# Kernel optimization log

Measured on AMD Instinct MI355X. Metric: run time of the kernel, lower is better.

Reference implementation:

```python
import jax, jax.numpy as jnp
import numpy as np

DIM = 1024
NUM_HEAD = 16
N_IMG = 64


def _linear_params(key, scale=0.02):
    kw, kb = jax.random.split(key)
    W = jax.random.normal(kw, (DIM, DIM), jnp.float32) * scale
    b = jax.random.normal(kb, (DIM,), jnp.float32) * scale
    return W, b


def setup_inputs() -> dict:
    key = jax.random.key(0)
    ks = jax.random.split(key, 5)
    # ragged per-image instance counts: 128..254, deterministic, sum = 12224
    lens = (128 + 2 * np.arange(N_IMG)).astype(np.int64)
    N = int(lens.sum())  # 12224
    x = jax.random.normal(ks[0], (N, DIM), jnp.float32)
    Wq, bq = _linear_params(ks[1])
    Wk, bk = _linear_params(ks[2])
    Wv, bv = _linear_params(ks[3])
    Wu, bu = _linear_params(ks[4])
    return {"x": x, "Wq": Wq, "bq": bq, "Wk": Wk, "bk": bk,
            "Wv": Wv, "bv": bv, "Wu": Wu, "bu": bu,
            "num_inst_per_image": jnp.asarray(lens)}


def _segment_layout(num_inst_per_image):
    # static (int) metadata -> numpy; returns padded gather idx, key mask, unpad idx
    lens = np.asarray(num_inst_per_image)
    B = lens.shape[0]
    L = int(lens.max())
    offsets = np.concatenate([[0], np.cumsum(lens)[:-1]])
    pos = offsets[:, None] + np.arange(L)[None, :]           # [B, L] flat positions
    valid = np.arange(L)[None, :] < lens[:, None]            # [B, L]
    gather_idx = jnp.asarray(np.where(valid, pos, 0))        # safe gather
    flat_take = jnp.asarray(np.flatnonzero(valid.ravel()))   # [N] unpad (row-major = segment order)
    return gather_idx, jnp.asarray(valid), flat_take, B, L


def reference(x, Wq, bq, Wk, bk, Wv, bv, Wu, bu, num_inst_per_image):
    gather_idx, valid, flat_take, B, L = _segment_layout(num_inst_per_image)
    N, C = x.shape
    H = NUM_HEAD
    D = C // H
    # global QKV projections on the flat batch (as in the torch module)
    q = (x @ Wq + bq)[gather_idx].reshape(B, L, H, D)
    k = (x @ Wk + bk)[gather_idx].reshape(B, L, H, D)
    v = (x @ Wv + bv)[gather_idx].reshape(B, L, H, D)
    scale = 1.0 / np.sqrt(C)  # note: original divides by sqrt(C), not sqrt(head_dim)
    attn = jnp.einsum('bqhd,bkhd->bhqk', q, k) * scale       # [B, H, L, L]
    bias = jnp.where(valid[:, None, None, :], 0.0, -jnp.inf)  # mask padded keys
    attn = jax.nn.softmax(attn + bias, axis=-1)
    out = jnp.einsum('bhqk,bkhd->bqhd', attn, v).reshape(B * L, C)
    out = out[flat_take]                                      # unpad back to [N, C]
    return out @ Wu + bu
```

## Files before the change

### kernel.cpp

```cpp
#include <hip/hip_runtime.h>
#include <hip/hip_bf16.h>
#include <math.h>

#define DIMC 1024
#define NHEAD 16
#define HDIM 64
#define MPAD 12288

using bf16x8 = __attribute__((ext_vector_type(8))) short;
using f32x4  = __attribute__((ext_vector_type(4))) float;
using f32x16 = __attribute__((ext_vector_type(16))) float;

__device__ inline ushort f2bf(float f) {
    uint u = __float_as_uint(f);
    u += 0x7fffu + ((u >> 16) & 1u);
    return (ushort)(u >> 16);
}
__device__ inline float bf2f(ushort h) { return __uint_as_float(((uint)h) << 16); }

__device__ inline uint pkbf(float a, float b) {
    __hip_bfloat162 t = __float22bfloat162_rn(float2{a, b});
    return *reinterpret_cast<uint*>(&t);
}

__device__ inline void gload_lds16(const ushort* g, ushort* l) {
    __builtin_amdgcn_global_load_lds(
        (const __attribute__((address_space(1))) uint*)g,
        (__attribute__((address_space(3))) uint*)l, 16, 0, 0);
}

__global__ __launch_bounds__(512, 2) void gemm192(
    const ushort* __restrict__ A, const ushort* __restrict__ Bt,
    const float* __restrict__ bq, const float* __restrict__ bk,
    const float* __restrict__ bv,
    ushort* __restrict__ qb, ushort* __restrict__ kb, ushort* __restrict__ vb,
    int M)
{
    __shared__ ushort lds[2][(256 + 192) * 64];

    const int bid = blockIdx.x;
    const int xcd = bid & 7;
    const int j   = bid >> 3;
    const int mt  = xcd * 6 + (j % 6);
    const int nt  = j / 6;
    const int row0 = mt * 256;
    const int col0 = nt * 192;

    const int t512 = threadIdx.x;
    const int w    = t512 >> 6;
    const int lane = t512 & 63;
    const int wm   = w >> 2;
    const int wn   = w & 3;
    const int l15  = lane & 15;
    const int kh   = lane >> 4;

    auto stage = [&](int buf, int kt, int mat, int relRow) {
        const int o   = relRow * 128 + lane * 16;
        const int row = o >> 7;
        const int kb_ = (o & 127) ^ ((row & 7) << 4);
        const ushort* src = (mat ? Bt + (size_t)(col0 + row) * DIMC
                                 : A  + (size_t)(row0 + row) * DIMC)
                            + kt * 64 + (kb_ >> 1);
        gload_lds16(src, &lds[buf][0] + mat * (256 * 64) + relRow * 64);
    };
    auto rdA = [&](int buf, int qr, int fr, int ks) -> bf16x8 {
        const int row = wm * 128 + qr * 64 + fr * 16 + l15;
        const int ad  = (row * 128 + ks * 64 + kh * 16) ^ ((row & 7) << 4);
        return *(const bf16x8*)(&lds[buf][0] + (ad >> 1));
    };
    auto rdB = [&](int buf, int n, int ks) -> bf16x8 {
        const int row = wn * 48 + n * 16 + l15;
        const int ad  = (row * 128 + ks * 64 + kh * 16) ^ ((row & 7) << 4);
        return *(const bf16x8*)(&lds[buf][256 * 64] + (ad >> 1));
    };

    f32x4 acc[8][3] = {};
    bf16x8 af[4][2];
    bf16x8 bf[3][2];

    stage(0, 0, 0, wm * 128 + wn * 16);
    stage(0, 0, 0, wm * 128 + wn * 16 + 8);
    stage(0, 0, 1, wn * 48 + wm * 16);
    stage(0, 0, 1, wn * 48 + wm * 16 + 8);
    stage(0, 0, 1, wn * 48 + 32 + wm * 8);
    stage(0, 0, 0, wm * 128 + 64 + wn * 16);
    stage(0, 0, 0, wm * 128 + 64 + wn * 16 + 8);

    const int NT = DIMC / 64;
    for (int t = 0; t < NT; ++t) {
        const int cur = t & 1;
        const int nxt = cur ^ 1;
        const int tn  = (t + 1 < NT) ? (t + 1) : (NT - 1);

        asm volatile("s_waitcnt vmcnt(3)" ::: "memory");
        __builtin_amdgcn_s_barrier();
        __builtin_amdgcn_sched_barrier(0);
        #pragma unroll
        for (int fr = 0; fr < 4; ++fr)
            #pragma unroll
            for (int ks = 0; ks < 2; ++ks)
                af[fr][ks] = rdA(cur, 0, fr, ks);
        #pragma unroll
        for (int n = 0; n < 2; ++n)
            #pragma unroll
            for (int ks = 0; ks < 2; ++ks)
                bf[n][ks] = rdB(cur, n, ks);
        stage(nxt, tn, 0, wm * 128 + wn * 16);
        stage(nxt, tn, 0, wm * 128 + wn * 16 + 8);
        stage(nxt, tn, 1, wn * 48 + wm * 16);
        stage(nxt, tn, 1, wn * 48 + wm * 16 + 8);
        __builtin_amdgcn_s_setprio(1);
        #pragma unroll
        for (int fr = 0; fr < 4; ++fr)
            #pragma unroll
            for (int n = 0; n < 2; ++n)
                #pragma unroll
                for (int ks = 0; ks < 2; ++ks)
                    acc[fr][n] = __builtin_amdgcn_mfma_f32_16x16x32_bf16(
                        af[fr][ks], bf[n][ks], acc[fr][n], 0, 0, 0);
        __builtin_amdgcn_s_setprio(0);

        asm volatile("s_waitcnt vmcnt(6)" ::: "memory");
        __builtin_amdgcn_s_barrier();
        __builtin_amdgcn_sched_barrier(0);
        #pragma unroll
        for (int ks = 0; ks < 2; ++ks)
            bf[2][ks] = rdB(cur, 2, ks);
        stage(nxt, tn, 1, wn * 48 + 32 + wm * 8);
        __builtin_amdgcn_s_setprio(1);
        #pragma unroll
        for (int fr = 0; fr < 4; ++fr)
            #pragma unroll
            for (int ks = 0; ks < 2; ++ks)
                acc[fr][2] = __builtin_amdgcn_mfma_f32_16x16x32_bf16(
                    af[fr][ks], bf[2][ks], acc[fr][2], 0, 0, 0);
        __builtin_amdgcn_s_setprio(0);

        asm volatile("s_waitcnt vmcnt(5)" ::: "memory");
        __builtin_amdgcn_s_barrier();
        __builtin_amdgcn_sched_barrier(0);
        #pragma unroll
        for (int fr = 0; fr < 4; ++fr)
            #pragma unroll
            for (int ks = 0; ks < 2; ++ks)
                af[fr][ks] = rdA(cur, 1, fr, ks);
        stage(nxt, tn, 0, wm * 128 + 64 + wn * 16);
        stage(nxt, tn, 0, wm * 128 + 64 + wn * 16 + 8);
        __builtin_amdgcn_s_setprio(1);
        #pragma unroll
        for (int fr = 0; fr < 4; ++fr)
            #pragma unroll
            for (int n = 0; n < 3; ++n)
                #pragma unroll
                for (int ks = 0; ks < 2; ++ks)
                    acc[4 + fr][n] = __builtin_amdgcn_mfma_f32_16x16x32_bf16(
                        af[fr][ks], bf[n][ks], acc[4 + fr][n], 0, 0, 0);
        __builtin_amdgcn_s_setprio(0);
    }

    #pragma unroll
    for (int n = 0; n < 3; ++n) {
        const int cg = col0 + wn * 48 + n * 16 + l15;
        const int s  = cg >> 10;
        const int cb = cg & 1023;
        const float bb = ((s == 0) ? bq : (s == 1) ? bk : bv)[cb];
        ushort* op     = (s == 0) ? qb : (s == 1) ? kb : vb;
        #pragma unroll
        for (int i = 0; i < 8; ++i) {
            #pragma unroll
            for (int r = 0; r < 4; ++r) {
                const int gr = row0 + wm * 128 + i * 16 + kh * 4 + r;
                if (gr < M)
                    op[(size_t)gr * DIMC + cb] = f2bf(acc[i][n][r] + bb);
            }
        }
    }
}

__global__ __launch_bounds__(512, 2) void gemm256f(
    const ushort* __restrict__ A, const ushort* __restrict__ Bt,
    const float* __restrict__ bias, float* __restrict__ C, int M)
{
    __shared__ ushort lds[2][2][256 * 64];

    const int bid = blockIdx.x;
    const int xcd = bid & 7;
    const int j   = bid >> 3;
    const int mt  = xcd * 6 + (j % 6);
    const int nt  = j / 6;
    const int row0 = mt * 256;
    const int col0 = nt * 256;

    const int t512 = threadIdx.x;
    const int w    = t512 >> 6;
    const int lane = t512 & 63;
    const int wm   = w >> 2;
    const int wn   = w & 3;
    const int l15  = lane & 15;
    const int kh   = lane >> 4;

    auto stage = [&](int buf, int kt, int mat, int relRow) {
        const int o   = relRow * 128 + lane * 16;
        const int row = o >> 7;
        const int kb_ = (o & 127) ^ ((row & 7) << 4);
        const ushort* src = (mat ? Bt + (size_t)(col0 + row) * DIMC
                                 : A  + (size_t)(row0 + row) * DIMC)
                            + kt * 64 + (kb_ >> 1);
        gload_lds16(src, &lds[buf][mat][0] + relRow * 64);
    };
    auto rdA = [&](int buf, int qr, int fr, int ks) -> bf16x8 {
        const int row = wm * 128 + qr * 64 + fr * 16 + l15;
        const int ad  = (row * 128 + ks * 64 + kh * 16) ^ ((row & 7) << 4);
        return *(const bf16x8*)(&lds[buf][0][0] + (ad >> 1));
    };
    auto rdB = [&](int buf, int qc, int fc, int ks) -> bf16x8 {
        const int row = wn * 64 + qc * 32 + fc * 16 + l15;
        const int ad  = (row * 128 + ks * 64 + kh * 16) ^ ((row & 7) << 4);
        return *(const bf16x8*)(&lds[buf][1][0] + (ad >> 1));
    };

    f32x4 acc[8][4] = {};
    bf16x8 af[4][2];
    bf16x8 bq2[2][2][2];

    stage(0, 0, 0, wm * 128 + wn * 16);
    stage(0, 0, 0, wm * 128 + wn * 16 + 8);
    stage(0, 0, 1, wn * 64 + wm * 16);
    stage(0, 0, 1, wn * 64 + wm * 16 + 8);
    stage(0, 0, 1, wn * 64 + 32 + wm * 16);
    stage(0, 0, 1, wn * 64 + 32 + wm * 16 + 8);
    stage(0, 0, 0, wm * 128 + 64 + wn * 16);
    stage(0, 0, 0, wm * 128 + 64 + wn * 16 + 8);

    const int NT = DIMC / 64;
    for (int t = 0; t < NT; ++t) {
        const int cur = t & 1;
        const int nxt = cur ^ 1;
        const int tn  = (t + 1 < NT) ? (t + 1) : (NT - 1);

        asm volatile("s_waitcnt vmcnt(4)" ::: "memory");
        __builtin_amdgcn_s_barrier();
        __builtin_amdgcn_sched_barrier(0);
        #pragma unroll
        for (int fr = 0; fr < 4; ++fr)
            #pragma unroll
            for (int ks = 0; ks < 2; ++ks)
                af[fr][ks] = rdA(cur, 0, fr, ks);
        #pragma unroll
        for (int fc = 0; fc < 2; ++fc)
            #pragma unroll
            for (int ks = 0; ks < 2; ++ks)
                bq2[0][fc][ks] = rdB(cur, 0, fc, ks);
        stage(nxt, tn, 0, wm * 128 + wn * 16);
        stage(nxt, tn, 0, wm * 128 + wn * 16 + 8);
        stage(nxt, tn, 1, wn * 64 + wm * 16);
        stage(nxt, tn, 1, wn * 64 + wm * 16 + 8);
        __builtin_amdgcn_s_setprio(1);
        #pragma unroll
        for (int fr = 0; fr < 4; ++fr)
            #pragma unroll
            for (int fc = 0; fc < 2; ++fc)
                #pragma unroll
                for (int ks = 0; ks < 2; ++ks)
                    acc[fr][fc] = __builtin_amdgcn_mfma_f32_16x16x32_bf16(
                        af[fr][ks], bq2[0][fc][ks], acc[fr][fc], 0, 0, 0);
        __builtin_amdgcn_s_setprio(0);

        asm volatile("s_waitcnt vmcnt(6)" ::: "memory");
        __builtin_amdgcn_s_barrier();
        __builtin_amdgcn_sched_barrier(0);
        #pragma unroll
        for (int fc = 0; fc < 2; ++fc)
            #pragma unroll
            for (int ks = 0; ks < 2; ++ks)
                bq2[1][fc][ks] = rdB(cur, 1, fc, ks);
        stage(nxt, tn, 1, wn * 64 + 32 + wm * 16);
        stage(nxt, tn, 1, wn * 64 + 32 + wm * 16 + 8);
        __builtin_amdgcn_s_setprio(1);
        #pragma unroll
        for (int fr = 0; fr < 4; ++fr)
            #pragma unroll
            for (int fc = 0; fc < 2; ++fc)
                #pragma unroll
                for (int ks = 0; ks < 2; ++ks)
                    acc[fr][2 + fc] = __builtin_amdgcn_mfma_f32_16x16x32_bf16(
                        af[fr][ks], bq2[1][fc][ks], acc[fr][2 + fc], 0, 0, 0);
        __builtin_amdgcn_s_setprio(0);

        asm volatile("s_waitcnt vmcnt(6)" ::: "memory");
        __builtin_amdgcn_s_barrier();
        __builtin_amdgcn_sched_barrier(0);
        #pragma unroll
        for (int fr = 0; fr < 4; ++fr)
            #pragma unroll
            for (int ks = 0; ks < 2; ++ks)
                af[fr][ks] = rdA(cur, 1, fr, ks);
        stage(nxt, tn, 0, wm * 128 + 64 + wn * 16);
        stage(nxt, tn, 0, wm * 128 + 64 + wn * 16 + 8);
        __builtin_amdgcn_s_setprio(1);
        #pragma unroll
        for (int fr = 0; fr < 4; ++fr)
            #pragma unroll
            for (int fc = 0; fc < 2; ++fc)
                #pragma unroll
                for (int ks = 0; ks < 2; ++ks)
                    acc[4 + fr][fc] = __builtin_amdgcn_mfma_f32_16x16x32_bf16(
                        af[fr][ks], bq2[0][fc][ks], acc[4 + fr][fc], 0, 0, 0);
        #pragma unroll
        for (int fr = 0; fr < 4; ++fr)
            #pragma unroll
            for (int fc = 0; fc < 2; ++fc)
                #pragma unroll
                for (int ks = 0; ks < 2; ++ks)
                    acc[4 + fr][2 + fc] = __builtin_amdgcn_mfma_f32_16x16x32_bf16(
                        af[fr][ks], bq2[1][fc][ks], acc[4 + fr][2 + fc], 0, 0, 0);
        __builtin_amdgcn_s_setprio(0);
    }

    #pragma unroll
    for (int n = 0; n < 4; ++n) {
        const int c  = col0 + wn * 64 + n * 16 + l15;
        const float bb = bias[c];
        #pragma unroll
        for (int i = 0; i < 8; ++i) {
            #pragma unroll
            for (int r = 0; r < 4; ++r) {
                const int gr = row0 + wm * 128 + i * 16 + kh * 4 + r;
                if (gr < M)
                    C[(size_t)gr * DIMC + c] = acc[i][n][r] + bb;
            }
        }
    }
}

__global__ __launch_bounds__(256) void cvt_pad(
    const float* __restrict__ x, ushort* __restrict__ xb, int nvalid, int ntot)
{
    const int stride = gridDim.x * blockDim.x;
    for (int i = blockIdx.x * blockDim.x + threadIdx.x; i < ntot / 4; i += stride) {
        const int e = i * 4;
        ushort4 o;
        if (e < nvalid) {
            const float4 f = *(const float4*)(x + e);
            o.x = f2bf(f.x); o.y = f2bf(f.y); o.z = f2bf(f.z); o.w = f2bf(f.w);
        } else { o.x = o.y = o.z = o.w = 0; }
        *(ushort4*)(xb + e) = o;
    }
}

__global__ __launch_bounds__(256) void transpose_w4(
    const float* __restrict__ W0, const float* __restrict__ W1,
    const float* __restrict__ W2, const float* __restrict__ W3,
    ushort* __restrict__ T0, ushort* __restrict__ T1,
    ushort* __restrict__ T2, ushort* __restrict__ T3)
{
    __shared__ float tile[32][33];
    const int z = blockIdx.z;
    const float* W = (z == 0) ? W0 : (z == 1) ? W1 : (z == 2) ? W2 : W3;
    ushort*      T = (z == 0) ? T0 : (z == 1) ? T1 : (z == 2) ? T2 : T3;
    const int tx = threadIdx.x & 31;
    const int ty = threadIdx.x >> 5;
    const int n0 = blockIdx.x * 32;
    const int k0 = blockIdx.y * 32;
    #pragma unroll
    for (int i = 0; i < 32; i += 8)
        tile[ty + i][tx] = W[(size_t)(k0 + ty + i) * DIMC + n0 + tx];
    __syncthreads();
    #pragma unroll
    for (int i = 0; i < 32; i += 8)
        T[(size_t)(n0 + ty + i) * DIMC + k0 + tx] = f2bf(tile[tx][ty + i]);
}

__global__ __launch_bounds__(64) void attn_mfma(
    const ushort* __restrict__ qg, const ushort* __restrict__ kg,
    const ushort* __restrict__ vg, ushort* __restrict__ og,
    const int* __restrict__ lens, int B)
{
    __shared__ ushort Vt[64 * 68];

    const int i   = blockIdx.x;
    const int xcd = i & 7;
    const int j   = i >> 3;
    const int bh  = xcd * (B * 2) + (j >> 2);
    const int qt  = j & 3;
    const int h   = bh & 15;
    const int b   = bh >> 4;

    const int lane = threadIdx.x & 63;

    const int myl = (lane < B) ? lens[lane] : 0;
    int inc = myl;
    #pragma unroll
    for (int d = 1; d < 64; d <<= 1) {
        const int nb = __shfl_up(inc, d);
        if (lane >= d) inc += nb;
    }
    const int off = __shfl(inc, b) - __shfl(myl, b);
    const int L   = __shfl(myl, b);
    if (qt * 64 >= L) return;
    const int ntk = (L + 63) >> 6;

    const int l31 = lane & 31;
    const int hi  = lane >> 5;
    const int kp  = lane & 31;
    const int dh  = lane >> 5;

    bf16x8 qf[2][4];
    #pragma unroll
    for (int qn = 0; qn < 2; ++qn) {
        const size_t row = (size_t)(off + min(qt * 64 + qn * 32 + l31, L - 1));
        #pragma unroll
        for (int ks = 0; ks < 4; ++ks) {
            union { uint4 u4; ushort us[8]; bf16x8 v; } tmp;
            tmp.u4 = *(const uint4*)(qg + row * DIMC + h * HDIM + ks * 16 + hi * 8);
            #pragma unroll
            for (int e = 0; e < 8; ++e)
                tmp.us[e] = f2bf(bf2f(tmp.us[e]) * 0.03125f);
            qf[qn][ks] = tmp.v;
        }
    }

    f32x16 o[2][2] = {};
    float mst[2] = {-1e30f, -1e30f};
    float lst[2] = {0.f, 0.f};

    uint4 va[4], vbr[4];
    auto issueV = [&](int tt) {
        const int j0s = tt * 64;
        #pragma unroll
        for (int it = 0; it < 4; ++it) {
            const int d0 = (it * 2 + dh) * 8;
            const size_t r0 = (size_t)(off + min(j0s + 2 * kp,     L - 1));
            const size_t r1 = (size_t)(off + min(j0s + 2 * kp + 1, L - 1));
            va[it]  = *(const uint4*)(vg + r0 * DIMC + h * HDIM + d0);
            vbr[it] = *(const uint4*)(vg + r1 * DIMC + h * HDIM + d0);
        }
    };

    bf16x8 kfc[2][4], kfn[2][4];
    auto loadK = [&](int tt, bf16x8 (&kf)[2][4]) {
        const int j0s = tt * 64;
        #pragma unroll
        for (int km = 0; km < 2; ++km) {
            const size_t row = (size_t)(off + min(j0s + km * 32 + l31, L - 1));
            #pragma unroll
            for (int ks = 0; ks < 4; ++ks)
                kf[km][ks] = *(const bf16x8*)(kg + row * DIMC + h * HDIM + ks * 16 + hi * 8);
        }
    };

    issueV(0);
    loadK(0, kfc);

    for (int t = 0; t < ntk; ++t) {
        const int j0 = t * 64;

        loadK(min(t + 1, ntk - 1), kfn);

        f32x16 s[2][2] = {};
        __builtin_amdgcn_s_setprio(1);
        #pragma unroll
        for (int km = 0; km < 2; ++km)
            #pragma unroll
            for (int qn = 0; qn < 2; ++qn)
                #pragma unroll
                for (int ks = 0; ks < 4; ++ks)
                    s[km][qn] = __builtin_amdgcn_mfma_f32_32x32x16_bf16(
                        kfc[km][ks], qf[qn][ks], s[km][qn], 0, 0, 0);
        __builtin_amdgcn_s_setprio(0);

        #pragma unroll
        for (int it = 0; it < 4; ++it) {
            const int d0 = (it * 2 + dh) * 8;
            const uint a4[4] = {va[it].x,  va[it].y,  va[it].z,  va[it].w};
            const uint b4[4] = {vbr[it].x, vbr[it].y, vbr[it].z, vbr[it].w};
            #pragma unroll
            for (int jj = 0; jj < 4; ++jj) {
                const uint lo  = (a4[jj] & 0xffffu) | (b4[jj] << 16);
                const uint hi2 = (a4[jj] >> 16) | (b4[jj] & 0xffff0000u);
                *(uint*)&Vt[(d0 + 2 * jj)     * 68 + 2 * kp] = lo;
                *(uint*)&Vt[(d0 + 2 * jj + 1) * 68 + 2 * kp] = hi2;
            }
        }
        if (t + 1 < ntk) issueV(t + 1);

        const bool fullTile = (j0 + 64 <= L);
        float tmv[2];
        #pragma unroll
        for (int qn = 0; qn < 2; ++qn) {
            float tm = -1e30f;
            if (fullTile) {
                #pragma unroll
                for (int km = 0; km < 2; ++km)
                    #pragma unroll
                    for (int r = 0; r < 16; ++r)
                        tm = fmaxf(tm, s[km][qn][r]);
            } else {
                #pragma unroll
                for (int km = 0; km < 2; ++km)
                    #pragma unroll
                    for (int r = 0; r < 16; ++r) {
                        const int key = j0 + km * 32 + (r & 3) + 8 * (r >> 2) + 4 * hi;
                        float sv = s[km][qn][r];
                        sv = (key < L) ? sv : -1e30f;
                        s[km][qn][r] = sv;
                        tm = fmaxf(tm, sv);
                    }
            }
            tm = fmaxf(tm, __shfl_xor(tm, 32));
            tmv[qn] = tm;
        }

        const bool need = (tmv[0] > mst[0] + 4.f) || (tmv[1] > mst[1] + 4.f);
        if (__any(need)) {
            #pragma unroll
            for (int qn = 0; qn < 2; ++qn) {
                const float nm = fmaxf(mst[qn], tmv[qn]);
                const float corr = __expf(mst[qn] - nm);
                mst[qn] = nm;
                lst[qn] *= corr;
                #pragma unroll
                for (int dm = 0; dm < 2; ++dm)
                    #pragma unroll
                    for (int r = 0; r < 16; ++r)
                        o[dm][qn][r] *= corr;
            }
        }
        #pragma unroll
        for (int qn = 0; qn < 2; ++qn) {
            float ls = 0.f;
            #pragma unroll
            for (int km = 0; km < 2; ++km)
                #pragma unroll
                for (int r = 0; r < 16; ++r) {
                    const float p = __expf(s[km][qn][r] - mst[qn]);
                    s[km][qn][r] = p;
                    ls += p;
                }
            ls += __shfl_xor(ls, 32);
            lst[qn] += ls;
        }

        #pragma unroll
        for (int kspv = 0; kspv < 4; ++kspv) {
            const int km = kspv >> 1;
            const int sb = kspv & 1;

            bf16x8 Afr[2];
            #pragma unroll
            for (int dm = 0; dm < 2; ++dm) {
                const int d = dm * 32 + l31;
                const uint2 p0 = *(const uint2*)&Vt[d * 68 + kspv * 16 + hi * 8];
                const uint2 p1 = *(const uint2*)&Vt[d * 68 + kspv * 16 + hi * 8 + 4];
                union { uint u[4]; bf16x8 v; } aa;
                aa.u[0] = p0.x; aa.u[1] = p0.y; aa.u[2] = p1.x; aa.u[3] = p1.y;
                Afr[dm] = aa.v;
            }

            bf16x8 Bfr[2];
            #pragma unroll
            for (int qn = 0; qn < 2; ++qn) {
                const uint X0 = pkbf(s[km][qn][8 * sb + 0], s[km][qn][8 * sb + 1]);
                const uint X1 = pkbf(s[km][qn][8 * sb + 2], s[km][qn][8 * sb + 3]);
                const uint Y0 = pkbf(s[km][qn][8 * sb + 4], s[km][qn][8 * sb + 5]);
                const uint Y1 = pkbf(s[km][qn][8 * sb + 6], s[km][qn][8 * sb + 7]);
                const uint sx0 = (uint)__shfl_xor((int)X0, 32);
                const uint sx1 = (uint)__shfl_xor((int)X1, 32);
                const uint sy0 = (uint)__shfl_xor((int)Y0, 32);
                const uint sy1 = (uint)__shfl_xor((int)Y1, 32);
                union { uint u[4]; bf16x8 v; } bb;
                bb.u[0] = hi ? sy0 : X0;
                bb.u[1] = hi ? sy1 : X1;
                bb.u[2] = hi ? Y0 : sx0;
                bb.u[3] = hi ? Y1 : sx1;
                Bfr[qn] = bb.v;
            }

            __builtin_amdgcn_s_setprio(1);
            #pragma unroll
            for (int dm = 0; dm < 2; ++dm)
                #pragma unroll
                for (int qn = 0; qn < 2; ++qn)
                    o[dm][qn] = __builtin_amdgcn_mfma_f32_32x32x16_bf16(
                        Afr[dm], Bfr[qn], o[dm][qn], 0, 0, 0);
            __builtin_amdgcn_s_setprio(0);
        }

        #pragma unroll
        for (int km = 0; km < 2; ++km)
            #pragma unroll
            for (int ks = 0; ks < 4; ++ks)
                kfc[km][ks] = kfn[km][ks];
    }

    #pragma unroll
    for (int qn = 0; qn < 2; ++qn) {
        const int q = qt * 64 + qn * 32 + l31;
        if (q < L) {
            const float inv = 1.f / lst[qn];
            ushort* orow = og + (size_t)(off + q) * DIMC + h * HDIM;
            #pragma unroll
            for (int dm = 0; dm < 2; ++dm)
                #pragma unroll
                for (int bq2 = 0; bq2 < 4; ++bq2) {
                    const int r0 = 4 * bq2;
                    uint2 st;
                    st.x = pkbf(o[dm][qn][r0 + 0] * inv, o[dm][qn][r0 + 1] * inv);
                    st.y = pkbf(o[dm][qn][r0 + 2] * inv, o[dm][qn][r0 + 3] * inv);
                    *(uint2*)(orow + dm * 32 + 8 * bq2 + 4 * hi) = st;
                }
        }
    }
}

extern "C" void kernel_launch(void* const* d_in, const int* in_sizes, int n_in,
                              void* d_out, int out_size, void* d_ws, size_t ws_size,
                              hipStream_t stream)
{
    const float* x   = (const float*)d_in[0];
    const float* Wq  = (const float*)d_in[1];
    const float* bq  = (const float*)d_in[2];
    const float* Wk  = (const float*)d_in[3];
    const float* bk  = (const float*)d_in[4];
    const float* Wv  = (const float*)d_in[5];
    const float* bv  = (const float*)d_in[6];
    const float* Wu  = (const float*)d_in[7];
    const float* bu  = (const float*)d_in[8];
    const int*  lens = (const int*)d_in[9];

    const int N = in_sizes[0] / DIMC;
    const int B = in_sizes[9];

    ushort* xb  = (ushort*)d_ws;
    ushort* wtq = xb  + (size_t)MPAD * DIMC;
    ushort* wtk = wtq + (size_t)DIMC * DIMC;
    ushort* wtv = wtk + (size_t)DIMC * DIMC;
    ushort* wtu = wtv + (size_t)DIMC * DIMC;
    ushort* kb  = wtu + (size_t)DIMC * DIMC;
    ushort* vb  = kb  + (size_t)N * DIMC;
    ushort* qb  = (ushort*)d_out;
    ushort* ob  = xb;

    cvt_pad<<<2048, 256, 0, stream>>>(x, xb, N * DIMC, MPAD * DIMC);
    transpose_w4<<<dim3(32, 32, 4), 256, 0, stream>>>(Wq, Wk, Wv, Wu,
                                                      wtq, wtk, wtv, wtu);

    gemm192<<<768, 512, 0, stream>>>(xb, wtq, bq, bk, bv, qb, kb, vb, N);

    attn_mfma<<<dim3(B * NHEAD * 4), dim3(64), 0, stream>>>(qb, kb, vb, ob, lens, B);

    gemm256f<<<192, 512, 0, stream>>>(ob, wtu, bu, (float*)d_out, N);
}
```

Measured before the change: 234.9 us.

## Retile output GEMM to 192x256 tiles and merge QKV GEMM B-phases

The output-projection GEMM moves from 256x256 tiles on 192 blocks to 192x256 tiles on 256 blocks, so every CU on the device gets a block while LDS staging and fragment loads are reworked to fit. The QKV GEMM folds its second B-column phase into the first, which removes one barrier and one waitcnt per k-step. The retiling trades per-block reuse for better CU coverage. The merged phase issues more loads before the MFMAs start and holds more B fragments in registers at once.

After: 229.0 us. 2.5% less time.

```diff
diff --git a/kernel.cpp b/kernel.cpp
--- a/kernel.cpp
+++ b/kernel.cpp
@@ -92,7 +92,7 @@
         const int nxt = cur ^ 1;
         const int tn  = (t + 1 < NT) ? (t + 1) : (NT - 1);
 
-        asm volatile("s_waitcnt vmcnt(3)" ::: "memory");
+        asm volatile("s_waitcnt vmcnt(2)" ::: "memory");
         __builtin_amdgcn_s_barrier();
         __builtin_amdgcn_sched_barrier(0);
         #pragma unroll
@@ -101,7 +101,7 @@
             for (int ks = 0; ks < 2; ++ks)
                 af[fr][ks] = rdA(cur, 0, fr, ks);
         #pragma unroll
-        for (int n = 0; n < 2; ++n)
+        for (int n = 0; n < 3; ++n)
             #pragma unroll
             for (int ks = 0; ks < 2; ++ks)
                 bf[n][ks] = rdB(cur, n, ks);
@@ -109,31 +109,16 @@
         stage(nxt, tn, 0, wm * 128 + wn * 16 + 8);
         stage(nxt, tn, 1, wn * 48 + wm * 16);
         stage(nxt, tn, 1, wn * 48 + wm * 16 + 8);
+        stage(nxt, tn, 1, wn * 48 + 32 + wm * 8);
         __builtin_amdgcn_s_setprio(1);
         #pragma unroll
         for (int fr = 0; fr < 4; ++fr)
             #pragma unroll
-            for (int n = 0; n < 2; ++n)
+            for (int n = 0; n < 3; ++n)
                 #pragma unroll
                 for (int ks = 0; ks < 2; ++ks)
                     acc[fr][n] = __builtin_amdgcn_mfma_f32_16x16x32_bf16(
                         af[fr][ks], bf[n][ks], acc[fr][n], 0, 0, 0);
-        __builtin_amdgcn_s_setprio(0);
-
-        asm volatile("s_waitcnt vmcnt(6)" ::: "memory");
-        __builtin_amdgcn_s_barrier();
-        __builtin_amdgcn_sched_barrier(0);
-        #pragma unroll
-        for (int ks = 0; ks < 2; ++ks)
-            bf[2][ks] = rdB(cur, 2, ks);
-        stage(nxt, tn, 1, wn * 48 + 32 + wm * 8);
-        __builtin_amdgcn_s_setprio(1);
-        #pragma unroll
-        for (int fr = 0; fr < 4; ++fr)
-            #pragma unroll
-            for (int ks = 0; ks < 2; ++ks)
-                acc[fr][2] = __builtin_amdgcn_mfma_f32_16x16x32_bf16(
-                    af[fr][ks], bf[2][ks], acc[fr][2], 0, 0, 0);
         __builtin_amdgcn_s_setprio(0);
 
         asm volatile("s_waitcnt vmcnt(5)" ::: "memory");
@@ -177,18 +162,18 @@
     }
 }
 
-__global__ __launch_bounds__(512, 2) void gemm256f(
+__global__ __launch_bounds__(512, 2) void gemmF(
     const ushort* __restrict__ A, const ushort* __restrict__ Bt,
     const float* __restrict__ bias, float* __restrict__ C, int M)
 {
-    __shared__ ushort lds[2][2][256 * 64];
+    __shared__ ushort lds[2][(192 + 256) * 64];
 
     const int bid = blockIdx.x;
     const int xcd = bid & 7;
     const int j   = bid >> 3;
-    const int mt  = xcd * 6 + (j % 6);
-    const int nt  = j / 6;
-    const int row0 = mt * 256;
+    const int mt  = xcd * 8 + (j % 8);
+    const int nt  = j / 8;
+    const int row0 = mt * 192;
     const int col0 = nt * 256;
 
     const int t512 = threadIdx.x;
@@ -199,6 +184,8 @@
     const int l15  = lane & 15;
     const int kh   = lane >> 4;
 
+    const int awbase = (w & 4) ? (96 + (w - 4) * 8) : (w * 8);
+
     auto stage = [&](int buf, int kt, int mat, int relRow) {
         const int o   = relRow * 128 + lane * 16;
         const int row = o >> 7;
@@ -206,31 +193,30 @@
         const ushort* src = (mat ? Bt + (size_t)(col0 + row) * DIMC
                                  : A  + (size_t)(row0 + row) * DIMC)
                             + kt * 64 + (kb_ >> 1);
-        gload_lds16(src, &lds[buf][mat][0] + relRow * 64);
-    };
-    auto rdA = [&](int buf, int qr, int fr, int ks) -> bf16x8 {
-        const int row = wm * 128 + qr * 64 + fr * 16 + l15;
+        gload_lds16(src, &lds[buf][0] + mat * (192 * 64) + relRow * 64);
+    };
+    auto rdA = [&](int buf, int fr, int ks) -> bf16x8 {
+        const int row = wm * 96 + fr * 16 + l15;
         const int ad  = (row * 128 + ks * 64 + kh * 16) ^ ((row & 7) << 4);
-        return *(const bf16x8*)(&lds[buf][0][0] + (ad >> 1));
-    };
-    auto rdB = [&](int buf, int qc, int fc, int ks) -> bf16x8 {
-        const int row = wn * 64 + qc * 32 + fc * 16 + l15;
+        return *(const bf16x8*)(&lds[buf][0] + (ad >> 1));
+    };
+    auto rdB = [&](int buf, int n, int ks) -> bf16x8 {
+        const int row = wn * 64 + n * 16 + l15;
         const int ad  = (row * 128 + ks * 64 + kh * 16) ^ ((row & 7) << 4);
-        return *(const bf16x8*)(&lds[buf][1][0] + (ad >> 1));
-    };
-
-    f32x4 acc[8][4] = {};
-    bf16x8 af[4][2];
-    bf16x8 bq2[2][2][2];
-
-    stage(0, 0, 0, wm * 128 + wn * 16);
-    stage(0, 0, 0, wm * 128 + wn * 16 + 8);
-    stage(0, 0, 1, wn * 64 + wm * 16);
-    stage(0, 0, 1, wn * 64 + wm * 16 + 8);
-    stage(0, 0, 1, wn * 64 + 32 + wm * 16);
-    stage(0, 0, 1, wn * 64 + 32 + wm * 16 + 8);
-    stage(0, 0, 0, wm * 128 + 64 + wn * 16);
-    stage(0, 0, 0, wm * 128 + 64 + wn * 16 + 8);
+        return *(const bf16x8*)(&lds[buf][192 * 64] + (ad >> 1));
+    };
+
+    f32x4 acc[6][4] = {};
+    bf16x8 af[2][2];
+    bf16x8 bf[4][2];
+
+    stage(0, 0, 1, w * 32);
+    stage(0, 0, 1, w * 32 + 8);
+    stage(0, 0, 1, w * 32 + 16);
+    stage(0, 0, 1, w * 32 + 24);
+    stage(0, 0, 0, awbase);
+    stage(0, 0, 0, awbase + 32);
+    stage(0, 0, 0, awbase + 64);
 
     const int NT = DIMC / 64;
     for (int t = 0; t < NT; ++t) {
@@ -238,82 +224,73 @@
         const int nxt = cur ^ 1;
         const int tn  = (t + 1 < NT) ? (t + 1) : (NT - 1);
 
-        asm volatile("s_waitcnt vmcnt(4)" ::: "memory");
+        asm volatile("s_waitcnt vmcnt(2)" ::: "memory");
         __builtin_amdgcn_s_barrier();
         __builtin_amdgcn_sched_barrier(0);
         #pragma unroll
-        for (int fr = 0; fr < 4; ++fr)
+        for (int fr = 0; fr < 2; ++fr)
             #pragma unroll
             for (int ks = 0; ks < 2; ++ks)
-                af[fr][ks] = rdA(cur, 0, fr, ks);
-        #pragma unroll
-        for (int fc = 0; fc < 2; ++fc)
+                af[fr][ks] = rdA(cur, fr, ks);
+        #pragma unroll
+        for (int n = 0; n < 4; ++n)
             #pragma unroll
             for (int ks = 0; ks < 2; ++ks)
-                bq2[0][fc][ks] = rdB(cur, 0, fc, ks);
-        stage(nxt, tn, 0, wm * 128 + wn * 16);
-        stage(nxt, tn, 0, wm * 128 + wn * 16 + 8);
-        stage(nxt, tn, 1, wn * 64 + wm * 16);
-        stage(nxt, tn, 1, wn * 64 + wm * 16 + 8);
+                bf[n][ks] = rdB(cur, n, ks);
+        stage(nxt, tn, 1, w * 32);
+        stage(nxt, tn, 1, w * 32 + 8);
+        stage(nxt, tn, 1, w * 32 + 16);
+        stage(nxt, tn, 1, w * 32 + 24);
+        stage(nxt, tn, 0, awbase);
         __builtin_amdgcn_s_setprio(1);
         #pragma unroll
-        for (int fr = 0; fr < 4; ++fr)
-            #pragma unroll
-            for (int fc = 0; fc < 2; ++fc)
+        for (int fr = 0; fr < 2; ++fr)
+            #pragma unroll
+            for (int n = 0; n < 4; ++n)
                 #pragma unroll
                 for (int ks = 0; ks < 2; ++ks)
-                    acc[fr][fc] = __builtin_amdgcn_mfma_f32_16x16x32_bf16(
-                        af[fr][ks], bq2[0][fc][ks], acc[fr][fc], 0, 0, 0);
+                    acc[fr][n] = __builtin_amdgcn_mfma_f32_16x16x32_bf16(
+                        af[fr][ks], bf[n][ks], acc[fr][n], 0, 0, 0);
         __builtin_amdgcn_s_setprio(0);
 
         asm volatile("s_waitcnt vmcnt(6)" ::: "memory");
         __builtin_amdgcn_s_barrier();
         __builtin_amdgcn_sched_barrier(0);
         #pragma unroll
-        for (int fc = 0; fc < 2; ++fc)
+        for (int fr = 0; fr < 2; ++fr)
             #pragma unroll
             for (int ks = 0; ks < 2; ++ks)
-                bq2[1][fc][ks] = rdB(cur, 1, fc, ks);
-        stage(nxt, tn, 1, wn * 64 + 32 + wm * 16);
-        stage(nxt, tn, 1, wn * 64 + 32 + wm * 16 + 8);
+                af[fr][ks] = rdA(cur, 2 + fr, ks);
+        stage(nxt, tn, 0, awbase + 32);
         __builtin_amdgcn_s_setprio(1);
         #pragma unroll
-        for (int fr = 0; fr < 4; ++fr)
-            #pragma unroll
-            for (int fc = 0; fc < 2; ++fc)
+        for (int fr = 0; fr < 2; ++fr)
+            #pragma unroll
+            for (int n = 0; n < 4; ++n)
                 #pragma unroll
                 for (int ks = 0; ks < 2; ++ks)
-                    acc[fr][2 + fc] = __builtin_amdgcn_mfma_f32_16x16x32_bf16(
-                        af[fr][ks], bq2[1][fc][ks], acc[fr][2 + fc], 0, 0, 0);
+                    acc[2 + fr][n] = __builtin_amdgcn_mfma_f32_16x16x32_bf16(
+                        af[fr][ks], bf[n][ks], acc[2 + fr][n], 0, 0, 0);
         __builtin_amdgcn_s_setprio(0);
 
         asm volatile("s_waitcnt vmcnt(6)" ::: "memory");
         __builtin_amdgcn_s_barrier();
         __builtin_amdgcn_sched_barrier(0);
         #pragma unroll
-        for (int fr = 0; fr < 4; ++fr)
+        for (int fr = 0; fr < 2; ++fr)
             #pragma unroll
             for (int ks = 0; ks < 2; ++ks)
-                af[fr][ks] = rdA(cur, 1, fr, ks);
-        stage(nxt, tn, 0, wm * 128 + 64 + wn * 16);
-        stage(nxt, tn, 0, wm * 128 + 64 + wn * 16 + 8);
+                af[fr][ks] = rdA(cur, 4 + fr, ks);
+        stage(nxt, tn, 0, awbase + 64);
         __builtin_amdgcn_s_setprio(1);
         #pragma unroll
-        for (int fr = 0; fr < 4; ++fr)
-            #pragma unroll
-            for (int fc = 0; fc < 2; ++fc)
+        for (int fr = 0; fr < 2; ++fr)
+            #pragma unroll
+            for (int n = 0; n < 4; ++n)
                 #pragma unroll
                 for (int ks = 0; ks < 2; ++ks)
-                    acc[4 + fr][fc] = __builtin_amdgcn_mfma_f32_16x16x32_bf16(
-                        af[fr][ks], bq2[0][fc][ks], acc[4 + fr][fc], 0, 0, 0);
-        #pragma unroll
-        for (int fr = 0; fr < 4; ++fr)
-            #pragma unroll
-            for (int fc = 0; fc < 2; ++fc)
-                #pragma unroll
-                for (int ks = 0; ks < 2; ++ks)
-                    acc[4 + fr][2 + fc] = __builtin_amdgcn_mfma_f32_16x16x32_bf16(
-                        af[fr][ks], bq2[1][fc][ks], acc[4 + fr][2 + fc], 0, 0, 0);
+                    acc[4 + fr][n] = __builtin_amdgcn_mfma_f32_16x16x32_bf16(
+                        af[fr][ks], bf[n][ks], acc[4 + fr][n], 0, 0, 0);
         __builtin_amdgcn_s_setprio(0);
     }
 
@@ -322,10 +299,10 @@
         const int c  = col0 + wn * 64 + n * 16 + l15;
         const float bb = bias[c];
         #pragma unroll
-        for (int i = 0; i < 8; ++i) {
+        for (int i = 0; i < 6; ++i) {
             #pragma unroll
             for (int r = 0; r < 4; ++r) {
-                const int gr = row0 + wm * 128 + i * 16 + kh * 4 + r;
+                const int gr = row0 + wm * 96 + i * 16 + kh * 4 + r;
                 if (gr < M)
                     C[(size_t)gr * DIMC + c] = acc[i][n][r] + bb;
             }
@@ -649,5 +626,5 @@
 
     attn_mfma<<<dim3(B * NHEAD * 4), dim3(64), 0, stream>>>(qb, kb, vb, ob, lens, B);
 
-    gemm256f<<<192, 512, 0, stream>>>(ob, wtu, bu, (float*)d_out, N);
-}
+    gemmF<<<256, 512, 0, stream>>>(ob, wtu, bu, (float*)d_out, N);
+}
```
